# Kernel tuning notes

Hardware: AMD Instinct MI355X
Metric: run time of the kernel (lower is better)

The kernel has to match this reference:

```python
import jax, jax.numpy as jnp
import numpy as np

# Config (matches init_kwargs)
B, L, D = 2, 2048, 1024
QH, KVH, HD, FFN = 8, 2, 128, 4096
EPS = 1.1920929e-07  # torch RMSNorm default eps = finfo(float32).eps


def _rope_ts():
    d2 = HD // 2
    freq_exp = (2.0 / HD) * jnp.arange(d2, dtype=jnp.float32)
    return 10000.0 ** freq_exp  # [d2]


def _rope(x):
    # x: [B, L, H, HD], rotated in fp32 (matches x.float() in source)
    d2 = HD // 2
    pos = jnp.arange(L, dtype=jnp.float32)
    rad = pos[:, None] / _rope_ts()[None, :]          # [L, d2]
    s = jnp.sin(rad)[None, :, None, :]                # [1, L, 1, d2]
    c = jnp.cos(rad)[None, :, None, :]
    xf = x.astype(jnp.float32)
    x1, x2 = xf[..., :d2], xf[..., d2:]
    return jnp.concatenate([x1 * c - x2 * s, x2 * c + x1 * s], axis=-1).astype(x.dtype)


def _rmsnorm(x, w):
    xf = x.astype(jnp.float32)
    r = jax.lax.rsqrt(jnp.mean(xf * xf, axis=-1, keepdims=True) + EPS)
    return (xf * r).astype(x.dtype) * w


def setup_inputs() -> dict:
    key = jax.random.key(0)
    ks = jax.random.split(key, 9)
    s = 0.02
    return {
        "x": jax.random.normal(ks[0], (B, L, D), dtype=jnp.float32),
        "ln1_w": jnp.ones((D,), dtype=jnp.float32),
        "wq": jax.random.normal(ks[1], (D, QH * HD), dtype=jnp.float32) * s,
        "wk": jax.random.normal(ks[2], (D, KVH * HD), dtype=jnp.float32) * s,
        "wv": jax.random.normal(ks[3], (D, KVH * HD), dtype=jnp.float32) * s,
        "wo": jax.random.normal(ks[4], (QH * HD, D), dtype=jnp.float32) * s,
        "ln2_w": jnp.ones((D,), dtype=jnp.float32),
        "wg": jax.random.normal(ks[5], (D, FFN), dtype=jnp.float32) * s,
        "wu": jax.random.normal(ks[6], (D, FFN), dtype=jnp.float32) * s,
        "wd": jax.random.normal(ks[7], (FFN, D), dtype=jnp.float32) * s,
    }


def reference(x, ln1_w, wq, wk, wv, wo, ln2_w, wg, wu, wd):
    residual = x
    h = _rmsnorm(x, ln1_w)

    q = _rope((h @ wq).reshape(B, L, QH, HD))          # [B,L,QH,HD]
    k = _rope((h @ wk).reshape(B, L, KVH, HD))         # [B,L,KVH,HD]
    v = (h @ wv).reshape(B, L, KVH, HD)

    rep = QH // KVH  # kv_map = floor(arange(QH)*KVH/QH) == repeat each kv head `rep` times
    qh = jnp.transpose(q, (0, 2, 1, 3)).astype(jnp.float32)                       # [B,QH,L,HD]
    kh = jnp.transpose(jnp.repeat(k, rep, axis=2), (0, 2, 1, 3)).astype(jnp.float32)
    vh = jnp.transpose(jnp.repeat(v, rep, axis=2), (0, 2, 1, 3)).astype(jnp.float32)

    scores = jnp.einsum("bhqd,bhkd->bhqk", qh, kh) / jnp.sqrt(jnp.float32(HD))    # [B,QH,L,L]
    causal = jnp.triu(jnp.ones((L, L), dtype=bool), 1)
    scores = jnp.where(causal, -jnp.inf, scores)
    attn = jax.nn.softmax(scores, axis=-1)
    ctx = jnp.einsum("bhqk,bhkd->bhqd", attn, vh)                                 # [B,QH,L,HD]
    ctx = jnp.transpose(ctx, (0, 2, 1, 3)).reshape(B, L, QH * HD).astype(x.dtype)

    x = ctx @ wo + residual
    residual = x
    h = _rmsnorm(x, ln2_w)
    return (jax.nn.silu(h @ wg) * (h @ wu)) @ wd + residual
```

## Files before the change

### kernel.cpp

```cpp
#include <hip/hip_runtime.h>
#include <hip/hip_bf16.h>
#include <math.h>

#define B_ 2
#define L_ 2048
#define D_ 1024
#define QH_ 8
#define KVH_ 2
#define HD_ 128
#define FFN_ 4096
#define T_ (B_ * L_)
#define EPS_ 1.1920929e-07f

typedef __bf16 bf16x8 __attribute__((ext_vector_type(8)));
typedef float floatx4 __attribute__((ext_vector_type(4)));
typedef unsigned short ushortx8 __attribute__((ext_vector_type(8)));
typedef unsigned short ushortx4 __attribute__((ext_vector_type(4)));

__device__ __forceinline__ unsigned short f2bf(float f) {
  union { float f; unsigned int u; } v;
  v.f = f;
  unsigned int r = v.u + 0x7FFFu + ((v.u >> 16) & 1u);
  return (unsigned short)(r >> 16);
}
__device__ __forceinline__ float bf2f(unsigned short u) {
  union { unsigned int u; float f; } v;
  v.u = ((unsigned int)u) << 16;
  return v.f;
}
__device__ __forceinline__ void gload_lds16(const void* g, void* l) {
  __builtin_amdgcn_global_load_lds((const __attribute__((address_space(1))) void*)g,
                                   (__attribute__((address_space(3))) void*)l, 16, 0, 0);
}

__device__ __forceinline__ void strip_tc(const float* __restrict__ in,
                                         unsigned short* __restrict__ out,
                                         int K, int N, int n0, int k0) {
  __shared__ float tile[4][32][33];
  int t = threadIdx.x;
  int tx = t & 31, ty = t >> 5;
#pragma unroll
  for (int s = 0; s < 4; s++)
#pragma unroll
    for (int r0 = 0; r0 < 4; r0++) {
      int r = ty + r0 * 8;
      tile[s][r][tx] = in[(size_t)(k0 + s * 32 + r) * N + n0 + tx];
    }
  __syncthreads();
  int nr = t >> 3, kq = t & 7;
#pragma unroll
  for (int s = 0; s < 4; s++) {
    ushortx4 o4;
#pragma unroll
    for (int j = 0; j < 4; j++) o4[j] = f2bf(tile[s][kq * 4 + j][nr]);
    *(ushortx4*)(out + (size_t)(n0 + nr) * K + k0 + s * 32 + kq * 4) = o4;
  }
}

__device__ __forceinline__ void rmsnorm_row(const float* __restrict__ x,
                                            const float* __restrict__ w,
                                            unsigned short* __restrict__ o, int row) {
  __shared__ float red[4];
  int t = threadIdx.x;
  const float* xr = x + (size_t)row * D_;
  float4 xv = *(const float4*)(xr + t * 4);
  float ss = xv.x * xv.x + xv.y * xv.y + xv.z * xv.z + xv.w * xv.w;
#pragma unroll
  for (int off = 32; off >= 1; off >>= 1) ss += __shfl_xor(ss, off);
  if ((t & 63) == 0) red[t >> 6] = ss;
  __syncthreads();
  float total = red[0] + red[1] + red[2] + red[3];
  float r = rsqrtf(total * (1.0f / (float)D_) + EPS_);
  float4 wv = *(const float4*)(w + t * 4);
  unsigned short* op = o + (size_t)row * D_ + t * 4;
  op[0] = f2bf(xv.x * r * wv.x);
  op[1] = f2bf(xv.y * r * wv.y);
  op[2] = f2bf(xv.z * r * wv.z);
  op[3] = f2bf(xv.w * r * wv.w);
}

__global__ __launch_bounds__(256) void prep_all(
    const float* __restrict__ wq, const float* __restrict__ wk,
    const float* __restrict__ wv, const float* __restrict__ wo,
    const float* __restrict__ wg, const float* __restrict__ wu,
    const float* __restrict__ wd, unsigned short* __restrict__ wT,
    const float* __restrict__ x, const float* __restrict__ ln1w,
    unsigned short* __restrict__ h_bf) {
  int bid = blockIdx.x;
  if (bid < 3712) {
    const float* in;
    unsigned short* out;
    int K, N, nt, base;
    if (bid < 256)       { in = wq; out = wT;            K = 1024; N = 1024; nt = 32;  base = 0; }
    else if (bid < 320)  { in = wk; out = wT + 1048576;  K = 1024; N = 256;  nt = 8;   base = 256; }
    else if (bid < 384)  { in = wv; out = wT + 1310720;  K = 1024; N = 256;  nt = 8;   base = 320; }
    else if (bid < 640)  { in = wo; out = wT + 1572864;  K = 1024; N = 1024; nt = 32;  base = 384; }
    else if (bid < 1664) { in = wg; out = wT + 2621440;  K = 1024; N = 4096; nt = 128; base = 640; }
    else if (bid < 2688) { in = wu; out = wT + 6815744;  K = 1024; N = 4096; nt = 128; base = 1664; }
    else                 { in = wd; out = wT + 11010048; K = 4096; N = 1024; nt = 32;  base = 2688; }
    int idx = bid - base;
    strip_tc(in, out, K, N, (idx % nt) * 32, (idx / nt) * 128);
  } else {
    rmsnorm_row(x, ln1w, h_bf, bid - 3712);
  }
}

__global__ __launch_bounds__(256) void rmsnorm_bf16_kernel(const float* __restrict__ x,
                                                           const float* __restrict__ w,
                                                           unsigned short* __restrict__ o) {
  rmsnorm_row(x, w, o, blockIdx.x);
}

template <int EPI, int KH>
__global__ __launch_bounds__(256, 3) void gemm_bf16(const unsigned short* __restrict__ A,
                                                    const unsigned short* __restrict__ BT,
                                                    const float* __restrict__ R,
                                                    float* __restrict__ C,
                                                    int M, int N, int K) {
  __shared__ unsigned short As[KH][64 * 32];
  __shared__ unsigned short Bs[KH][128 * 32];
  int t = threadIdx.x;
  int lane = t & 63, wave = t >> 6;
  int m0 = blockIdx.y * 64, n0 = blockIdx.x * 128;

  int row_a = t >> 2;
  int kc = ((t & 3) ^ ((t >> 3) & 3)) * 8;
  const unsigned short* ga0 = A + (size_t)(m0 + row_a) * K + kc;
  const unsigned short* gb0 = BT + (size_t)(n0 + row_a) * K + kc;
  const unsigned short* gb1 = BT + (size_t)(n0 + 64 + row_a) * K + kc;

  int wm = (wave & 1) * 32, wn = (wave >> 1) * 64;
  int fr = lane & 15, quad = lane >> 4;
  int sw = (quad ^ ((fr >> 1) & 3)) * 8;

  floatx4 acc[2][4];
#pragma unroll
  for (int i = 0; i < 2; i++)
#pragma unroll
    for (int j = 0; j < 4; j++) acc[i][j] = (floatx4){0.f, 0.f, 0.f, 0.f};

  for (int k0 = 0; k0 < K; k0 += 32 * KH) {
#pragma unroll
    for (int h = 0; h < KH; h++) {
      int ko = k0 + h * 32;
      gload_lds16(ga0 + ko, As[h] + wave * 512);
      gload_lds16(gb0 + ko, Bs[h] + wave * 512);
      gload_lds16(gb1 + ko, Bs[h] + 2048 + wave * 512);
    }
    __syncthreads();
#pragma unroll
    for (int h = 0; h < KH; h++) {
      const unsigned short* arp = As[h] + (size_t)(wm + fr) * 32 + sw;
      const unsigned short* brp = Bs[h] + (size_t)(wn + fr) * 32 + sw;
      bf16x8 af[2], bfr[4];
#pragma unroll
      for (int i = 0; i < 2; i++)
        af[i] = __builtin_bit_cast(bf16x8, *(const ushortx8*)(arp + i * 16 * 32));
#pragma unroll
      for (int j = 0; j < 4; j++)
        bfr[j] = __builtin_bit_cast(bf16x8, *(const ushortx8*)(brp + j * 16 * 32));
#pragma unroll
      for (int i = 0; i < 2; i++)
#pragma unroll
        for (int j = 0; j < 4; j++)
          acc[i][j] = __builtin_amdgcn_mfma_f32_16x16x32_bf16(af[i], bfr[j], acc[i][j], 0, 0, 0);
    }
    __syncthreads();
  }

  int orow = m0 + wm + quad * 4;
  int ocol = n0 + wn + fr;
#pragma unroll
  for (int i = 0; i < 2; i++) {
#pragma unroll
    for (int r = 0; r < 4; r++) {
      int row = orow + i * 16 + r;
#pragma unroll
      for (int j = 0; j < 4; j++) {
        size_t idx = (size_t)row * N + ocol + j * 16;
        float v = acc[i][j][r];
        if (EPI == 1) C[idx] = v + R[idx];
        else C[idx] = v + C[idx];
      }
    }
  }
}

__global__ __launch_bounds__(256) void gemm_qkv(const unsigned short* __restrict__ A,
                                                const unsigned short* __restrict__ BT,
                                                unsigned short* __restrict__ qb,
                                                unsigned short* __restrict__ Kb,
                                                unsigned short* __restrict__ Vt) {
  constexpr int K = 1024;
  __shared__ unsigned short smem[24576];
  int t = threadIdx.x;
  int lane = t & 63, wave = t >> 6;
  int bx = blockIdx.x;
  int m0 = blockIdx.y * 64, n0 = bx * 128;

  int row_a = t >> 2;
  int kc = ((t & 3) ^ ((t >> 3) & 3)) * 8;
  const unsigned short* ga0 = A + (size_t)(m0 + row_a) * K + kc;
  const unsigned short* gb0 = BT + (size_t)(n0 + row_a) * K + kc;
  const unsigned short* gb1 = BT + (size_t)(n0 + 64 + row_a) * K + kc;

  int wm = (wave & 1) * 32, wn = (wave >> 1) * 64;
  int fr = lane & 15, quad = lane >> 4;
  int sw = (quad ^ ((fr >> 1) & 3)) * 8;

  floatx4 acc[2][4];
#pragma unroll
  for (int i = 0; i < 2; i++)
#pragma unroll
    for (int j = 0; j < 4; j++) acc[i][j] = (floatx4){0.f, 0.f, 0.f, 0.f};

  for (int k0 = 0; k0 < K; k0 += 128) {
#pragma unroll
    for (int h = 0; h < 4; h++) {
      int ko = k0 + h * 32;
      gload_lds16(ga0 + ko, smem + h * 2048 + wave * 512);
      gload_lds16(gb0 + ko, smem + 8192 + h * 4096 + wave * 512);
      gload_lds16(gb1 + ko, smem + 8192 + h * 4096 + 2048 + wave * 512);
    }
    __syncthreads();
#pragma unroll
    for (int h = 0; h < 4; h++) {
      const unsigned short* arp = smem + h * 2048 + (size_t)(wm + fr) * 32 + sw;
      const unsigned short* brp = smem + 8192 + h * 4096 + (size_t)(wn + fr) * 32 + sw;
      bf16x8 af[2], bfr[4];
#pragma unroll
      for (int i = 0; i < 2; i++)
        af[i] = __builtin_bit_cast(bf16x8, *(const ushortx8*)(arp + i * 16 * 32));
#pragma unroll
      for (int j = 0; j < 4; j++)
        bfr[j] = __builtin_bit_cast(bf16x8, *(const ushortx8*)(brp + j * 16 * 32));
#pragma unroll
      for (int i = 0; i < 2; i++)
#pragma unroll
        for (int j = 0; j < 4; j++)
          acc[i][j] = __builtin_amdgcn_mfma_f32_16x16x32_bf16(af[i], bfr[j], acc[i][j], 0, 0, 0);
    }
    __syncthreads();
  }

  unsigned short* scr = smem;
#pragma unroll
  for (int i = 0; i < 2; i++)
#pragma unroll
    for (int r = 0; r < 4; r++)
#pragma unroll
      for (int j = 0; j < 4; j++)
        scr[(size_t)(wm + quad * 4 + i * 16 + r) * 136 + wn + fr + j * 16] =
            f2bf(acc[i][j][r]);
  __syncthreads();

  if (bx < 10) {
    int row = t >> 2, dq = (t & 3) * 16;
    int tok = m0 + row, pos = tok & (L_ - 1), b = tok >> 11;
    float scale_ = (bx < 8) ? 0.08838834764831843f : 1.0f;
    unsigned short lo[16], hi[16];
#pragma unroll
    for (int m = 0; m < 16; m++) {
      int d2 = dq + m;
      float x1 = bf2f(scr[(size_t)row * 136 + d2]);
      float x2 = bf2f(scr[(size_t)row * 136 + d2 + 64]);
      float inv_ts = expf(-0.14391156831f * (float)d2);
      float rad = (float)pos * inv_ts;
      float s = sinf(rad), c = cosf(rad);
      lo[m] = f2bf((x1 * c - x2 * s) * scale_);
      hi[m] = f2bf((x2 * c + x1 * s) * scale_);
    }
    if (bx < 8) {
      unsigned short* dst = qb + (size_t)tok * 1024 + bx * 128;
      *(ushortx8*)(dst + dq) = *(const ushortx8*)(lo);
      *(ushortx8*)(dst + dq + 8) = *(const ushortx8*)(lo + 8);
      *(ushortx8*)(dst + 64 + dq) = *(const ushortx8*)(hi);
      *(ushortx8*)(dst + 64 + dq + 8) = *(const ushortx8*)(hi + 8);
    } else {
      int kvh = bx - 8, bk = b * KVH_ + kvh, swk = pos & 15;
      unsigned short* dst = Kb + ((size_t)bk * L_ + pos) * HD_;
      int c0 = dq >> 3;
      *(ushortx8*)(dst + ((c0) ^ swk) * 8) = *(const ushortx8*)(lo);
      *(ushortx8*)(dst + ((c0 + 1) ^ swk) * 8) = *(const ushortx8*)(lo + 8);
      *(ushortx8*)(dst + ((c0 + 8) ^ swk) * 8) = *(const ushortx8*)(hi);
      *(ushortx8*)(dst + ((c0 + 9) ^ swk) * 8) = *(const ushortx8*)(hi + 8);
    }
  } else {
    int kvh = bx - 10;
    int b = m0 >> 11, key0 = m0 & (L_ - 1), bk = b * KVH_ + kvh;
    int hd = t >> 1, half = t & 1;
#pragma unroll
    for (int c = 0; c < 4; c++) {
      int cp = half * 4 + c, kcc = cp ^ (hd & 7);
      ushortx8 ob;
#pragma unroll
      for (int j = 0; j < 8; j++) ob[j] = scr[(size_t)(kcc * 8 + j) * 136 + hd];
      *(ushortx8*)(Vt + ((size_t)bk * HD_ + hd) * L_ + key0 + cp * 8) = ob;
    }
  }
}

__global__ __launch_bounds__(512, 1) void gemm_gateup8p(
    const unsigned short* __restrict__ A,
    const unsigned short* __restrict__ BgT,
    const unsigned short* __restrict__ BuT,
    unsigned short* __restrict__ Cb) {
  constexpr int K = 1024;
  __shared__ unsigned short As[2][2][8192];
  __shared__ unsigned short Bs[2][2][8192];

  int t = threadIdx.x;
  int lane = t & 63, wave = t >> 6;
  int m0 = blockIdx.y * 256;
  int n0l = blockIdx.x * 128;

  int row_s = t >> 2;
  int kc = ((t & 3) ^ ((t >> 3) & 3)) * 8;
  const unsigned short* gaB[2];
  gaB[0] = A + (size_t)(m0 + row_s) * K + kc;
  gaB[1] = A + (size_t)(m0 + 128 + row_s) * K + kc;
  const unsigned short* gbB[2];
#pragma unroll
  for (int hf = 0; hf < 2; hf++) {
    int rb = hf * 128 + row_s;
    const unsigned short* src = ((rb & 31) < 16) ? BgT : BuT;
    gbB[hf] = src + (size_t)(n0l + (rb >> 5) * 16 + (rb & 15)) * K + kc;
  }

  int wm = wave >> 2, wn = wave & 3;
  int fr = lane & 15, quad = lane >> 4;
  int sw = (quad ^ ((fr >> 1) & 3)) * 8;
  int aro = (wm * 128 + fr) * 32 + sw;
  int bro = (wn * 64 + fr) * 32 + sw;

  floatx4 acc[8][4];
#pragma unroll
  for (int i = 0; i < 8; i++)
#pragma unroll
    for (int j = 0; j < 4; j++) acc[i][j] = (floatx4){0.f, 0.f, 0.f, 0.f};

  bf16x8 af[4][2], b0[2][2], b1[2][2];

#define GU_LDA(buf_, ilo_)                                                        \
  { _Pragma("unroll") for (int i_ = 0; i_ < 4; i_++) {                            \
      af[i_][0] = __builtin_bit_cast(                                             \
          bf16x8, *(const ushortx8*)(&As[buf_][0][aro + ((ilo_) + i_) * 512]));   \
      af[i_][1] = __builtin_bit_cast(                                             \
          bf16x8, *(const ushortx8*)(&As[buf_][1][aro + ((ilo_) + i_) * 512])); } }

#define GU_LDB(buf_, jlo_, bp_)                                                   \
  { _Pragma("unroll") for (int j_ = 0; j_ < 2; j_++) {                            \
      bp_[j_][0] = __builtin_bit_cast(                                            \
          bf16x8, *(const ushortx8*)(&Bs[buf_][0][bro + ((jlo_) + j_) * 512]));   \
      bp_[j_][1] = __builtin_bit_cast(                                            \
          bf16x8, *(const ushortx8*)(&Bs[buf_][1][bro + ((jlo_) + j_) * 512])); } }

#define GU_MM(ilo_, jlo_, bp_)                                                    \
  { __builtin_amdgcn_s_setprio(1);                                                \
    _Pragma("unroll") for (int i_ = 0; i_ < 4; i_++)                              \
        _Pragma("unroll") for (int j_ = 0; j_ < 2; j_++) {                        \
      acc[(ilo_) + i_][(jlo_) + j_] = __builtin_amdgcn_mfma_f32_16x16x32_bf16(    \
          af[i_][0], bp_[j_][0], acc[(ilo_) + i_][(jlo_) + j_], 0, 0, 0);         \
      acc[(ilo_) + i_][(jlo_) + j_] = __builtin_amdgcn_mfma_f32_16x16x32_bf16(    \
          af[i_][1], bp_[j_][1], acc[(ilo_) + i_][(jlo_) + j_], 0, 0, 0); }       \
    __builtin_amdgcn_s_setprio(0); }

#define GU_STA(buf_, tile_, half_)                                                \
  { const unsigned short* g_ = gaB[half_] + (size_t)(tile_) * 64;                 \
    gload_lds16(g_, &As[buf_][0][(half_) * 4096 + wave * 512]);                   \
    gload_lds16(g_ + 32, &As[buf_][1][(half_) * 4096 + wave * 512]); }

#define GU_STB(buf_, tile_, half_)                                                \
  { const unsigned short* g_ = gbB[half_] + (size_t)(tile_) * 64;                 \
    gload_lds16(g_, &Bs[buf_][0][(half_) * 4096 + wave * 512]);                   \
    gload_lds16(g_ + 32, &Bs[buf_][1][(half_) * 4096 + wave * 512]); }

#define GU_BAR __builtin_amdgcn_s_barrier()
#define GU_LGKM0 asm volatile("s_waitcnt lgkmcnt(0)" ::: "memory")
#define GU_VM4 asm volatile("s_waitcnt vmcnt(4)" ::: "memory")
#define GU_VM0 asm volatile("s_waitcnt vmcnt(0)" ::: "memory")

  GU_STB(0, 0, 0); GU_STB(0, 0, 1);
  GU_STA(0, 0, 0); GU_STA(0, 0, 1);
  GU_STB(1, 1, 0); GU_STB(1, 1, 1);
  GU_VM4;
  GU_BAR;

#pragma unroll 1
  for (int n = 0; n < 7; n++) {
    int tb = 2 * n + 1, t2 = 2 * n + 2, t3 = 2 * n + 3;
    GU_LDA(0, 0); GU_LDB(0, 0, b0); GU_STA(1, tb, 0);
    GU_BAR; GU_LGKM0; GU_MM(0, 0, b0); GU_BAR;
    GU_LDB(0, 2, b1); GU_STA(1, tb, 1);
    GU_BAR; GU_LGKM0; GU_MM(0, 2, b1); GU_BAR;
    GU_LDA(0, 4); GU_STB(0, t2, 0);
    GU_BAR; GU_LGKM0; GU_MM(4, 0, b0); GU_BAR;
    GU_STB(0, t2, 1);
    GU_VM4;
    GU_BAR; GU_LGKM0; GU_MM(4, 2, b1); GU_BAR;
    GU_LDA(1, 0); GU_LDB(1, 0, b0); GU_STA(0, t2, 0);
    GU_BAR; GU_LGKM0; GU_MM(0, 0, b0); GU_BAR;
    GU_LDB(1, 2, b1); GU_STA(0, t2, 1);
    GU_BAR; GU_LGKM0; GU_MM(0, 2, b1); GU_BAR;
    GU_LDA(1, 4); GU_STB(1, t3, 0);
    GU_BAR; GU_LGKM0; GU_MM(4, 0, b0); GU_BAR;
    GU_STB(1, t3, 1);
    GU_VM4;
    GU_BAR; GU_LGKM0; GU_MM(4, 2, b1); GU_BAR;
  }
  GU_LDA(0, 0); GU_LDB(0, 0, b0); GU_STA(1, 15, 0);
  GU_BAR; GU_LGKM0; GU_MM(0, 0, b0); GU_BAR;
  GU_LDB(0, 2, b1); GU_STA(1, 15, 1);
  GU_BAR; GU_LGKM0; GU_MM(0, 2, b1); GU_BAR;
  GU_LDA(0, 4);
  GU_BAR; GU_LGKM0; GU_MM(4, 0, b0); GU_BAR;
  GU_VM0;
  GU_BAR; GU_LGKM0; GU_MM(4, 2, b1); GU_BAR;
  GU_LDA(1, 0); GU_LDB(1, 0, b0);
  GU_BAR; GU_LGKM0; GU_MM(0, 0, b0); GU_BAR;
  GU_LDB(1, 2, b1);
  GU_BAR; GU_LGKM0; GU_MM(0, 2, b1); GU_BAR;
  GU_LDA(1, 4);
  GU_BAR; GU_LGKM0; GU_MM(4, 0, b0); GU_BAR;
  GU_MM(4, 2, b1);

#undef GU_LDA
#undef GU_LDB
#undef GU_MM
#undef GU_STA
#undef GU_STB
#undef GU_BAR
#undef GU_LGKM0
#undef GU_VM4
#undef GU_VM0

#pragma unroll
  for (int i = 0; i < 8; i++) {
    int row = m0 + wm * 128 + i * 16 + quad * 4;
#pragma unroll
    for (int r = 0; r < 4; r++) {
#pragma unroll
      for (int jj = 0; jj < 2; jj++) {
        float g = acc[i][2 * jj][r];
        float u = acc[i][2 * jj + 1][r];
        int colL = n0l + (wn * 2 + jj) * 16 + fr;
        Cb[(size_t)(row + r) * FFN_ + colL] = f2bf(g / (1.f + __expf(-g)) * u);
      }
    }
  }
}

__global__ __launch_bounds__(256) void attn_mfma(const unsigned short* __restrict__ qb,
                                                 const unsigned short* __restrict__ Kb,
                                                 const unsigned short* __restrict__ Vt,
                                                 unsigned short* __restrict__ ctx) {
  __shared__ unsigned short Ks[64 * 128];
  __shared__ unsigned short Vs[128 * 64];
  __shared__ unsigned short Ps[4][16 * 72];
  int id = blockIdx.x;
  int bh = id & 15;
  int p_ = id >> 4;
  int qt = (p_ < 16) ? p_ : 47 - p_;
  int b = bh >> 3, h = bh & 7;
  int bk = b * KVH_ + (h >> 2);
  int q0 = qt * 64;
  int t = threadIdx.x, lane = t & 63, w = t >> 6;
  int fr = lane & 15, quad = lane >> 4;

  int pos = q0 + w * 16 + fr;
  const unsigned short* qrow = qb + (size_t)(b * L_ + pos) * 1024 + h * HD_;
  bf16x8 qf[4];
#pragma unroll
  for (int kb = 0; kb < 4; kb++)
    qf[kb] = __builtin_bit_cast(bf16x8, *(const ushortx8*)(qrow + kb * 32 + quad * 8));

  floatx4 o_acc[8];
#pragma unroll
  for (int nt = 0; nt < 8; nt++) o_acc[nt] = (floatx4){0.f, 0.f, 0.f, 0.f};
  float l_r[4] = {0.f, 0.f, 0.f, 0.f};
  unsigned short* Psw = Ps[w];
  const unsigned short* kgb = Kb + (size_t)bk * L_ * HD_;
  const unsigned short* vgb = Vt + (size_t)bk * HD_ * L_;
  int rowg0 = q0 + w * 16 + quad * 4;

  for (int kt = 0; kt <= qt; kt++) {
    int kstart = kt * 64;
    bool diag = (kt == qt);
    __syncthreads();
    const unsigned short* ksrc = kgb + (size_t)kstart * HD_;
#pragma unroll
    for (int it = 0; it < 4; it++) {
      int sl = it * 4 + w;
      gload_lds16(ksrc + sl * 512 + lane * 8, Ks + sl * 512);
    }
#pragma unroll
    for (int it = 0; it < 4; it++) {
      int sl = it * 4 + w;
      gload_lds16(vgb + (size_t)(sl * 8 + (lane >> 3)) * L_ + kstart + (lane & 7) * 8,
                  Vs + sl * 512);
    }
    __syncthreads();

    floatx4 s_acc[4];
#pragma unroll
    for (int jt = 0; jt < 4; jt++) s_acc[jt] = (floatx4){0.f, 0.f, 0.f, 0.f};
#pragma unroll
    for (int kb = 0; kb < 4; kb++) {
#pragma unroll
      for (int jt = 0; jt < 4; jt++) {
        bf16x8 kf = __builtin_bit_cast(
            bf16x8, *(const ushortx8*)(Ks + (jt * 16 + fr) * 128 +
                                       (((kb * 4 + quad) ^ fr) * 8)));
        s_acc[jt] = __builtin_amdgcn_mfma_f32_16x16x32_bf16(qf[kb], kf, s_acc[jt], 0, 0, 0);
      }
    }

#pragma unroll
    for (int jt = 0; jt < 4; jt++) {
#pragma unroll
      for (int r = 0; r < 4; r++) {
        float pp;
        if (diag) {
          int keyg = kstart + jt * 16 + fr;
          pp = (keyg <= rowg0 + r) ? __expf(s_acc[jt][r]) : 0.f;
        } else {
          pp = __expf(s_acc[jt][r]);
        }
        l_r[r] += pp;
        Psw[(quad * 4 + r) * 72 + jt * 16 + fr] = f2bf(pp);
      }
    }
    bf16x8 pf0 = __builtin_bit_cast(bf16x8, *(const ushortx8*)(Psw + fr * 72 + quad * 8));
    bf16x8 pf1 =
        __builtin_bit_cast(bf16x8, *(const ushortx8*)(Psw + fr * 72 + 32 + quad * 8));
#pragma unroll
    for (int nt = 0; nt < 8; nt++) {
      bf16x8 vf0 = __builtin_bit_cast(
          bf16x8,
          *(const ushortx8*)(Vs + (nt * 16 + fr) * 64 + ((quad ^ (fr & 7)) * 8)));
      bf16x8 vf1 = __builtin_bit_cast(
          bf16x8,
          *(const ushortx8*)(Vs + (nt * 16 + fr) * 64 + (((4 + quad) ^ (fr & 7)) * 8)));
      o_acc[nt] = __builtin_amdgcn_mfma_f32_16x16x32_bf16(pf0, vf0, o_acc[nt], 0, 0, 0);
      o_acc[nt] = __builtin_amdgcn_mfma_f32_16x16x32_bf16(pf1, vf1, o_acc[nt], 0, 0, 0);
    }
  }

#pragma unroll
  for (int r = 0; r < 4; r++) {
    l_r[r] += __shfl_xor(l_r[r], 1);
    l_r[r] += __shfl_xor(l_r[r], 2);
    l_r[r] += __shfl_xor(l_r[r], 4);
    l_r[r] += __shfl_xor(l_r[r], 8);
  }

  unsigned short* ob =
      ctx + (size_t)(b * L_ + q0 + w * 16 + quad * 4) * 1024 + h * HD_ + fr;
#pragma unroll
  for (int r = 0; r < 4; r++) {
    float inv = 1.f / l_r[r];
    unsigned short* orow = ob + (size_t)r * 1024;
#pragma unroll
    for (int nt = 0; nt < 8; nt++) orow[nt * 16] = f2bf(o_acc[nt][r] * inv);
  }
}

extern "C" void kernel_launch(void* const* d_in, const int* in_sizes, int n_in,
                              void* d_out, int out_size, void* d_ws, size_t ws_size,
                              hipStream_t stream) {
  const float* x    = (const float*)d_in[0];
  const float* ln1w = (const float*)d_in[1];
  const float* wq   = (const float*)d_in[2];
  const float* wk   = (const float*)d_in[3];
  const float* wvp  = (const float*)d_in[4];
  const float* wo   = (const float*)d_in[5];
  const float* ln2w = (const float*)d_in[6];
  const float* wg   = (const float*)d_in[7];
  const float* wu   = (const float*)d_in[8];
  const float* wd   = (const float*)d_in[9];
  float* out = (float*)d_out;
  char* ws = (char*)d_ws;

  unsigned short* wT = (unsigned short*)ws;
  unsigned short* wqkvT = wT;
  unsigned short* woT = wT + 1572864;
  unsigned short* wgT = wT + 2621440;
  unsigned short* wuT = wT + 6815744;
  unsigned short* wdT = wT + 11010048;
  unsigned short* h_bf = (unsigned short*)(ws + 30408704);
  unsigned short* qb = (unsigned short*)(ws + 38797312);
  unsigned short* h2_bf = (unsigned short*)(ws + 51380224);
  unsigned short* Kb = (unsigned short*)(ws + 59768832);
  unsigned short* Vt = (unsigned short*)(ws + 61865984);
  unsigned short* gu = (unsigned short*)(ws + 59768832);
  unsigned short* ctx_bf = h_bf;

  dim3 blk(256);

  prep_all<<<3712 + T_, blk, 0, stream>>>(wq, wk, wvp, wo, wg, wu, wd, wT, x, ln1w, h_bf);
  gemm_qkv<<<dim3(12, 64), blk, 0, stream>>>(h_bf, wqkvT, qb, Kb, Vt);
  attn_mfma<<<512, blk, 0, stream>>>(qb, Kb, Vt, ctx_bf);
  gemm_bf16<1, 4><<<dim3(8, 64), blk, 0, stream>>>(ctx_bf, woT, x, out, T_, 1024, 1024);
  rmsnorm_bf16_kernel<<<T_, blk, 0, stream>>>(out, ln2w, h2_bf);
  gemm_gateup8p<<<dim3(32, 16), dim3(512), 0, stream>>>(h2_bf, wgT, wuT, gu);
  gemm_bf16<2, 4><<<dim3(8, 64), blk, 0, stream>>>(gu, wdT, nullptr, out, T_, 1024, FFN_);
}
```

Measured before the change: 367.6 us.

## Remap gate/up GEMM blocks per XCD and issue A-tile loads earlier

```diff
diff --git a/kernel.cpp b/kernel.cpp
--- a/kernel.cpp
+++ b/kernel.cpp
@@ -311,8 +311,12 @@
 
   int t = threadIdx.x;
   int lane = t & 63, wave = t >> 6;
-  int m0 = blockIdx.y * 256;
-  int n0l = blockIdx.x * 128;
+  int bid = blockIdx.x;
+  int xcd = bid & 7, idx = bid >> 3;
+  int xb = xcd * 4 + (idx >> 4);
+  int yb = idx & 15;
+  int m0 = yb * 256;
+  int n0l = xb * 128;
 
   int row_s = t >> 2;
   int kc = ((t & 3) ^ ((t >> 3) & 3)) * 8;
@@ -377,40 +381,41 @@
 
 #define GU_BAR __builtin_amdgcn_s_barrier()
 #define GU_LGKM0 asm volatile("s_waitcnt lgkmcnt(0)" ::: "memory")
-#define GU_VM4 asm volatile("s_waitcnt vmcnt(4)" ::: "memory")
+#define GU_VM6 asm volatile("s_waitcnt vmcnt(6)" ::: "memory")
 #define GU_VM0 asm volatile("s_waitcnt vmcnt(0)" ::: "memory")
 
   GU_STB(0, 0, 0); GU_STB(0, 0, 1);
   GU_STA(0, 0, 0); GU_STA(0, 0, 1);
   GU_STB(1, 1, 0); GU_STB(1, 1, 1);
-  GU_VM4;
+  GU_STA(1, 1, 0);
+  GU_VM6;
   GU_BAR;
 
 #pragma unroll 1
   for (int n = 0; n < 7; n++) {
-    int tb = 2 * n + 1, t2 = 2 * n + 2, t3 = 2 * n + 3;
-    GU_LDA(0, 0); GU_LDB(0, 0, b0); GU_STA(1, tb, 0);
+    int tO = 2 * n + 1, tE2 = 2 * n + 2, tO2 = 2 * n + 3;
+    GU_LDA(0, 0); GU_LDB(0, 0, b0); GU_STA(1, tO, 1);
     GU_BAR; GU_LGKM0; GU_MM(0, 0, b0); GU_BAR;
-    GU_LDB(0, 2, b1); GU_STA(1, tb, 1);
+    GU_LDB(0, 2, b1);
     GU_BAR; GU_LGKM0; GU_MM(0, 2, b1); GU_BAR;
-    GU_LDA(0, 4); GU_STB(0, t2, 0);
+    GU_LDA(0, 4); GU_STB(0, tE2, 0);
     GU_BAR; GU_LGKM0; GU_MM(4, 0, b0); GU_BAR;
-    GU_STB(0, t2, 1);
-    GU_VM4;
+    GU_STB(0, tE2, 1); GU_STA(0, tE2, 0);
+    GU_VM6;
     GU_BAR; GU_LGKM0; GU_MM(4, 2, b1); GU_BAR;
-    GU_LDA(1, 0); GU_LDB(1, 0, b0); GU_STA(0, t2, 0);
+    GU_LDA(1, 0); GU_LDB(1, 0, b0); GU_STA(0, tE2, 1);
     GU_BAR; GU_LGKM0; GU_MM(0, 0, b0); GU_BAR;
-    GU_LDB(1, 2, b1); GU_STA(0, t2, 1);
+    GU_LDB(1, 2, b1);
     GU_BAR; GU_LGKM0; GU_MM(0, 2, b1); GU_BAR;
-    GU_LDA(1, 4); GU_STB(1, t3, 0);
+    GU_LDA(1, 4); GU_STB(1, tO2, 0);
     GU_BAR; GU_LGKM0; GU_MM(4, 0, b0); GU_BAR;
-    GU_STB(1, t3, 1);
-    GU_VM4;
+    GU_STB(1, tO2, 1); GU_STA(1, tO2, 0);
+    GU_VM6;
     GU_BAR; GU_LGKM0; GU_MM(4, 2, b1); GU_BAR;
   }
-  GU_LDA(0, 0); GU_LDB(0, 0, b0); GU_STA(1, 15, 0);
+  GU_LDA(0, 0); GU_LDB(0, 0, b0); GU_STA(1, 15, 1);
   GU_BAR; GU_LGKM0; GU_MM(0, 0, b0); GU_BAR;
-  GU_LDB(0, 2, b1); GU_STA(1, 15, 1);
+  GU_LDB(0, 2, b1);
   GU_BAR; GU_LGKM0; GU_MM(0, 2, b1); GU_BAR;
   GU_LDA(0, 4);
   GU_BAR; GU_LGKM0; GU_MM(4, 0, b0); GU_BAR;
@@ -431,7 +436,7 @@
 #undef GU_STB
 #undef GU_BAR
 #undef GU_LGKM0
-#undef GU_VM4
+#undef GU_VM6
 #undef GU_VM0
 
 #pragma unroll
@@ -602,6 +607,6 @@
   attn_mfma<<<512, blk, 0, stream>>>(qb, Kb, Vt, ctx_bf);
   gemm_bf16<1, 4><<<dim3(8, 64), blk, 0, stream>>>(ctx_bf, woT, x, out, T_, 1024, 1024);
   rmsnorm_bf16_kernel<<<T_, blk, 0, stream>>>(out, ln2w, h2_bf);
-  gemm_gateup8p<<<dim3(32, 16), dim3(512), 0, stream>>>(h2_bf, wgT, wuT, gu);
+  gemm_gateup8p<<<512, dim3(512), 0, stream>>>(h2_bf, wgT, wuT, gu);
   gemm_bf16<2, 4><<<dim3(8, 64), blk, 0, stream>>>(gu, wdT, nullptr, out, T_, 1024, FFN_);
 }
```

Result: no change. 366.1 us (-0.4%).
